# Kernel optimization log

Hardware: AMD Instinct MI355X
Metric: run time of the kernel (lower is better)

Reference implementation:

```python
import jax, jax.numpy as jnp
import numpy as np
from jax import lax

NUM_HEADS = 6
LN_EPS = 1e-5


def _ln(x, g, b):
    mu = jnp.mean(x, axis=-1, keepdims=True)
    var = jnp.mean(jnp.square(x - mu), axis=-1, keepdims=True)
    return (x - mu) * jax.lax.rsqrt(var + LN_EPS) * g + b


def _gelu(x):
    return jax.nn.gelu(x, approximate=False)


def setup_inputs() -> dict:
    key = jax.random.key(0)
    ks = jax.random.split(key, 16)
    B, N, C = 16, 1025, 384
    hid = 4 * C  # 1536
    k3 = 3  # depthwise kernel size
    s = 0.02
    rn = lambda k, shape: (jax.random.normal(k, shape, jnp.float32) * s)
    return {
        "x": jax.random.normal(ks[0], (B, N, C), jnp.float32),
        "ln1_g": jnp.ones((C,), jnp.float32),
        "ln1_b": jnp.zeros((C,), jnp.float32),
        "qkv_w": rn(ks[1], (3 * C, C)),
        "proj_w": rn(ks[2], (C, C)),
        "proj_b": jnp.zeros((C,), jnp.float32),
        "ln2_g": jnp.ones((C,), jnp.float32),
        "ln2_b": jnp.zeros((C,), jnp.float32),
        "conv1_w": rn(ks[3], (hid, C)),          # 1x1 conv as matrix
        "conv1_b": jnp.zeros((hid,), jnp.float32),
        "conv2_w": rn(ks[4], (hid, 1, k3, k3)),   # depthwise OIHW
        "conv2_b": jnp.zeros((hid,), jnp.float32),
        "conv3_w": rn(ks[5], (C, hid)),           # 1x1 conv as matrix
        "conv3_b": jnp.zeros((C,), jnp.float32),
        "bn1_s": jnp.ones((hid,), jnp.float32), "bn1_b": jnp.zeros((hid,), jnp.float32),
        "bn2_s": jnp.ones((hid,), jnp.float32), "bn2_b": jnp.zeros((hid,), jnp.float32),
        "bn3_s": jnp.ones((C,), jnp.float32), "bn3_b": jnp.zeros((C,), jnp.float32),
        "comp_w": rn(ks[6], (C // 4, C)), "comp_b": jnp.zeros((C // 4,), jnp.float32),
        "exc_w": rn(ks[7], (C, C // 4)), "exc_b": jnp.zeros((C,), jnp.float32),
    }


def _block(x, ln1_g, ln1_b, qkv_w, proj_w, proj_b, ln2_g, ln2_b,
           conv1_w, conv1_b, conv2_w, conv2_b, conv3_w, conv3_b,
           bn1_s, bn1_b, bn2_s, bn2_b, bn3_s, bn3_b,
           comp_w, comp_b, exc_w, exc_b):
    B, N, C = x.shape
    Hh = NUM_HEADS
    hd = C // Hh
    S = int(np.sqrt(N - 1))

    # ---- Attention (manual softmax(QK^T)V) ----
    h = _ln(x, ln1_g, ln1_b)
    qkv = jnp.einsum('bnc,dc->bnd', h, qkv_w).reshape(B, N, 3, Hh, hd)
    qkv = qkv.transpose(2, 0, 3, 1, 4)  # [3,B,H,N,hd]
    q, k, v = qkv[0], qkv[1], qkv[2]
    attn = jax.nn.softmax(jnp.einsum('bhqd,bhkd->bhqk', q, k) * (hd ** -0.5), axis=-1)
    o = jnp.einsum('bhqk,bhkd->bhqd', attn, v).transpose(0, 2, 1, 3).reshape(B, N, C)
    o = o @ proj_w.T + proj_b
    x = x + o

    # ---- DAFF FFN (conv + BN(eval affine) + GELU + SE gating on cls) ----
    h2 = _ln(x, ln2_g, ln2_b)
    cls_tok, tok = h2[:, :1], h2[:, 1:]
    t = tok.reshape(B, S, S, C).transpose(0, 3, 1, 2)  # NCHW
    hid = conv1_w.shape[0]
    y = jnp.einsum('bchw,oc->bohw', t, conv1_w) + conv1_b[None, :, None, None]
    y = y * bn1_s[None, :, None, None] + bn1_b[None, :, None, None]
    y = _gelu(y)
    shortcut = y
    y = lax.conv_general_dilated(y, conv2_w, (1, 1), 'SAME',
                                 feature_group_count=hid,
                                 dimension_numbers=('NCHW', 'OIHW', 'NCHW'))
    y = y + conv2_b[None, :, None, None]
    y = y * bn2_s[None, :, None, None] + bn2_b[None, :, None, None]
    y = shortcut + _gelu(y)
    y = jnp.einsum('bchw,oc->bohw', y, conv3_w) + conv3_b[None, :, None, None]
    y = y * bn3_s[None, :, None, None] + bn3_b[None, :, None, None]
    # SE gate on cls token
    w = jnp.mean(y, axis=(2, 3)).reshape(B, 1, C)
    w = _gelu(w @ comp_w.T + comp_b) @ exc_w.T + exc_b
    cls_out = cls_tok * w
    tok_out = y.reshape(B, C, S * S).transpose(0, 2, 1)
    out = jnp.concatenate([cls_out, tok_out], axis=1)
    return x + out


def reference(x, ln1_g, ln1_b, qkv_w, proj_w, proj_b, ln2_g, ln2_b,
              conv1_w, conv1_b, conv2_w, conv2_b, conv3_w, conv3_b,
              bn1_s, bn1_b, bn2_s, bn2_b, bn3_s, bn3_b,
              comp_w, comp_b, exc_w, exc_b):
    return _block(x, ln1_g, ln1_b, qkv_w, proj_w, proj_b, ln2_g, ln2_b,
                  conv1_w, conv1_b, conv2_w, conv2_b, conv3_w, conv3_b,
                  bn1_s, bn1_b, bn2_s, bn2_b, bn3_s, bn3_b,
                  comp_w, comp_b, exc_w, exc_b)
```

## Files before the change

### kernel.cpp

```cpp
#include <hip/hip_runtime.h>
#include <math.h>

#define DI __device__ __forceinline__

namespace {

constexpr int B_ = 16;
constexpr int N_ = 1025;
constexpr int C_ = 384;
constexpr int H_ = 6;
constexpr int HD_ = 64;
constexpr int HID_ = 1536;
constexpr int P_ = 1024;
constexpr int MTOK = B_ * P_;
constexpr int MALL = B_ * N_;
constexpr int NPAD = 1088;
constexpr long long AF = (long long)MALL * C_;

constexpr int NQKV = 3 * C_ * C_;
constexpr int NPROJ = C_ * C_;
constexpr int NC1 = HID_ * C_;
constexpr int NC3 = C_ * HID_;
constexpr int NW2 = HID_ * 9;
constexpr int T1 = NQKV, T2 = T1 + NPROJ, T3 = T2 + NC1, T4 = T3 + NC3;
constexpr int T5 = T4 + NW2, T6 = T5 + HID_;

typedef __attribute__((ext_vector_type(4))) float f32x4;
typedef __attribute__((ext_vector_type(16))) float f32x16;
typedef __attribute__((ext_vector_type(8))) short bf16x8;

DI float gelu_f(float x) { return 0.5f * x * (1.0f + erff(x * 0.7071067811865475f)); }

DI float us2f(unsigned short u) {
  union { unsigned int i; float f; } c; c.i = ((unsigned)u) << 16; return c.f;
}
DI unsigned short f2us(float f) {
  union { float f; unsigned int i; } c; c.f = f;
  unsigned int r = c.i + 0x7FFF + ((c.i >> 16) & 1);
  return (unsigned short)(r >> 16);
}
DI unsigned short f2us_trunc(float f) {
  union { float f; unsigned int i; } c; c.f = f;
  return (unsigned short)(c.i >> 16);
}
DI void bf8_to_f(const uint4 v, float* f) {
  const unsigned int u[4] = {v.x, v.y, v.z, v.w};
#pragma unroll
  for (int t = 0; t < 4; t++) {
    union { unsigned int i; float fl; } lo, hi;
    lo.i = (u[t] & 0xffffu) << 16;
    hi.i = u[t] & 0xffff0000u;
    f[2 * t] = lo.fl; f[2 * t + 1] = hi.fl;
  }
}
DI uint4 f_to_bf8(const float* f) {
  unsigned int w[4];
#pragma unroll
  for (int t = 0; t < 4; t++)
    w[t] = (unsigned)f2us(f[2 * t]) | ((unsigned)f2us(f[2 * t + 1]) << 16);
  return make_uint4(w[0], w[1], w[2], w[3]);
}

DI unsigned cvt_pk_bf16(float lo, float hi) {
  unsigned d;
  asm("v_cvt_pk_bf16_f32 %0, %1, %2" : "=v"(d) : "v"(lo), "v"(hi));
  return d;
}
DI void permswap(unsigned &a, unsigned &b) {
  asm("v_permlane32_swap_b32 %0, %1" : "+v"(a), "+v"(b));
}

DI void gl2lds16(const unsigned short* g, unsigned short* l) {
  __builtin_amdgcn_global_load_lds(
      (const __attribute__((address_space(1))) void*)g,
      (__attribute__((address_space(3))) void*)l, 16, 0, 0);
}

__global__ __launch_bounds__(256) void cvtall_kernel(
    const float* __restrict__ qkv_w, const float* __restrict__ proj_w,
    const float* __restrict__ conv1_w, const float* __restrict__ conv3_w,
    const float* __restrict__ conv2_w, const float* __restrict__ c2b,
    const float* __restrict__ s2, const float* __restrict__ b2,
    unsigned short* __restrict__ dst16, float* __restrict__ Bc)
{
  const int idx = blockIdx.x * 256 + threadIdx.x;
  if (idx < T1)      dst16[idx] = f2us(qkv_w[idx]);
  else if (idx < T2) dst16[idx] = f2us(proj_w[idx - T1]);
  else if (idx < T3) dst16[idx] = f2us(conv1_w[idx - T2]);
  else if (idx < T4) dst16[idx] = f2us(conv3_w[idx - T3]);
  else if (idx < T5) {
    const int r = idx - T4, tap = r / HID_, c = r % HID_;
    dst16[idx] = f2us(conv2_w[c * 9 + tap] * s2[c]);
  } else if (idx < T6) {
    const int c = idx - T5;
    Bc[c] = c2b[c] * s2[c] + b2[c];
  }
}

__global__ __launch_bounds__(256) void lnw_kernel(
    const float* __restrict__ x, const float* __restrict__ g,
    const float* __restrict__ b, unsigned short* __restrict__ out,
    float* __restrict__ cls_out, int nrows)
{
  const int row = blockIdx.x * 4 + (threadIdx.x >> 6);
  if (row >= nrows) return;
  const int lane = threadIdx.x & 63;
  const float* xr = x + (long long)row * C_;
  float v[6];
#pragma unroll
  for (int i = 0; i < 6; i++) v[i] = xr[lane + 64 * i];
  float s = 0.f, q = 0.f;
#pragma unroll
  for (int i = 0; i < 6; i++) { s += v[i]; q += v[i] * v[i]; }
#pragma unroll
  for (int m = 1; m < 64; m <<= 1) {
    s += __shfl_xor(s, m, 64);
    q += __shfl_xor(q, m, 64);
  }
  const float mean = s * (1.0f / C_);
  const float var  = q * (1.0f / C_) - mean * mean;
  const float rstd = rsqrtf(var + 1e-5f);
  unsigned short* orow = out + (long long)row * C_;
  const bool iscls = (cls_out != nullptr) && (row % N_) == 0;
  float* cr = iscls ? cls_out + (long long)(row / N_) * C_ : nullptr;
#pragma unroll
  for (int i = 0; i < 6; i++) {
    const int c = lane + 64 * i;
    const float r = (v[i] - mean) * rstd * g[c] + b[c];
    orow[c] = f2us(r);
    if (iscls) cr[c] = r;
  }
}

__global__ __launch_bounds__(256) void vtrans_kernel(
    const unsigned short* __restrict__ v, unsigned short* __restrict__ vt)
{
  __shared__ unsigned short t[64][72];
  const int bh = blockIdx.x, nt = blockIdx.y;
  const int n0 = nt * 64;
  const int tid = threadIdx.x;
  {
    const int nl = tid >> 2;
    const int dc = (tid & 3) * 16;
    const int gn = n0 + nl;
    uint4 a = make_uint4(0u,0u,0u,0u), b = make_uint4(0u,0u,0u,0u);
    if (gn < N_) {
      const unsigned short* p = v + ((long long)bh * N_ + gn) * HD_ + dc;
      a = *(const uint4*)p; b = *(const uint4*)(p + 8);
    }
    *(uint4*)&t[nl][dc] = a;
    *(uint4*)&t[nl][dc + 8] = b;
  }
  __syncthreads();
  {
    const int dl = tid >> 2;
    const int nc = (tid & 3) * 16;
    unsigned short tmp[16];
#pragma unroll
    for (int i = 0; i < 16; i++) tmp[i] = t[nc + i][dl];
    unsigned short* p = vt + ((long long)bh * HD_ + dl) * NPAD + n0 + nc;
    *(uint4*)p = *(uint4*)&tmp[0];
    *(uint4*)(p + 8) = *(uint4*)&tmp[8];
  }
}

enum { GM_QKV = 0, GM_PROJ = 1, GM_CONV1 = 2, GM_CONV3 = 3 };

template <int MODE, int K>
__global__ __launch_bounds__(256) void mgemm_kernel(
    const unsigned short* __restrict__ A, const unsigned short* __restrict__ W,
    void* __restrict__ o0, void* __restrict__ o1, void* __restrict__ o2,
    const float* __restrict__ e0, const float* __restrict__ e1,
    const float* __restrict__ e2, int M)
{
  __shared__ unsigned short As[2][128][64];
  __shared__ unsigned short Bs[2][128][64];
  const int m0 = blockIdx.x * 128, n0 = blockIdx.y * 128;
  if (m0 >= M) return;
  const int tid = threadIdx.x;
  const int lane = tid & 63, wv = tid >> 6;
  const int lane15 = lane & 15, quad = lane >> 4;
  const int wm = (wv >> 1) * 64, wn = (wv & 1) * 64;

  const unsigned short* agp[4];
  const unsigned short* bgp[4];
#pragma unroll
  for (int t = 0; t < 4; t++) {
    const int lr = wv * 32 + t * 8 + (lane >> 3);
    const int chunk = (lane & 7) ^ (lr & 7);
    int gm = m0 + lr;
    if (gm > M - 1) gm = M - 1;
    long long arow = gm;
    if constexpr (MODE == GM_CONV1) arow = (long long)(gm >> 10) * N_ + 1 + (gm & 1023);
    agp[t] = A + arow * K + chunk * 8;
    bgp[t] = W + (long long)(n0 + lr) * K + chunk * 8;
  }

  f32x4 acc[4][4];
#pragma unroll
  for (int i = 0; i < 4; i++)
#pragma unroll
    for (int j = 0; j < 4; j++) acc[i][j] = (f32x4)0.f;

  const int xsel = lane15 & 7;
  constexpr int NT = K / 64;

#pragma unroll
  for (int t = 0; t < 4; t++) {
    gl2lds16(agp[t], &As[0][wv * 32 + t * 8][0]);
    gl2lds16(bgp[t], &Bs[0][wv * 32 + t * 8][0]);
  }

  for (int it = 0; it < NT; ++it) {
    const int cur = it & 1;
    if (it + 1 < NT) {
      const int k0 = (it + 1) * 64;
#pragma unroll
      for (int t = 0; t < 4; t++) {
        gl2lds16(agp[t] + k0, &As[cur ^ 1][wv * 32 + t * 8][0]);
        gl2lds16(bgp[t] + k0, &Bs[cur ^ 1][wv * 32 + t * 8][0]);
      }
      asm volatile("s_waitcnt vmcnt(8)" ::: "memory");
    } else {
      asm volatile("s_waitcnt vmcnt(0)" ::: "memory");
    }
    asm volatile("s_barrier" ::: "memory");
    __builtin_amdgcn_sched_barrier(0);
#pragma unroll
    for (int kh = 0; kh < 2; kh++) {
      bf16x8 af[4], bfr[4];
#pragma unroll
      for (int i = 0; i < 4; i++)
        af[i] = *(const bf16x8*)&As[cur][wm + i * 16 + lane15][((kh * 4 + quad) ^ xsel) * 8];
#pragma unroll
      for (int j = 0; j < 4; j++)
        bfr[j] = *(const bf16x8*)&Bs[cur][wn + j * 16 + lane15][((kh * 4 + quad) ^ xsel) * 8];
#pragma unroll
      for (int i = 0; i < 4; i++)
#pragma unroll
        for (int j = 0; j < 4; j++)
          acc[i][j] = __builtin_amdgcn_mfma_f32_16x16x32_bf16(af[i], bfr[j], acc[i][j], 0, 0, 0);
    }
    asm volatile("s_barrier" ::: "memory");
  }
#pragma unroll
  for (int i = 0; i < 4; i++) {
#pragma unroll
    for (int r = 0; r < 4; r++) {
      const int m = m0 + wm + i * 16 + quad * 4 + r;
      if (m >= M) continue;
#pragma unroll
      for (int j = 0; j < 4; j++) {
        const int n = n0 + wn + j * 16 + lane15;
        const float val = acc[i][j][r];
        if constexpr (MODE == GM_QKV) {
          const int which = n / C_, rr = n % C_, hh = rr >> 6, e = rr & 63;
          const int b = m / N_, nn = m % N_;
          unsigned short* dst = (unsigned short*)((which == 0) ? o0 : ((which == 1) ? o1 : o2));
          const float sval = (which == 0) ? val * 0.18033688f : val;
          dst[(((long long)b * H_ + hh) * N_ + nn) * HD_ + e] = f2us(sval);
        } else if constexpr (MODE == GM_PROJ) {
          ((float*)o0)[(long long)m * C_ + n] = val + e0[(long long)m * C_ + n] + e1[n];
        } else if constexpr (MODE == GM_CONV1) {
          ((unsigned short*)o0)[(long long)m * HID_ + n] =
              f2us(gelu_f((val + e0[n]) * e1[n] + e2[n]));
        } else {
          const float val2 = (val + e0[n]) * e1[n] + e2[n];
          ((float*)o0)[(long long)m * C_ + n] = val2;
          const int bb = m >> 10, pp = m & 1023;
          const long long orow = ((long long)bb * N_ + 1 + pp) * C_ + n;
          ((float*)o1)[orow] = ((const float*)o2)[orow] + val2;
        }
      }
    }
  }
}

__global__ __launch_bounds__(512) void fattn_kernel(
    const unsigned short* __restrict__ q, const unsigned short* __restrict__ k,
    const unsigned short* __restrict__ vt, unsigned short* __restrict__ o)
{
  __shared__ unsigned short smem[32768];
  const int tid = threadIdx.x;
  const int lane = tid & 63, wv = tid >> 6;
  const int qw = wv & 3, kg = wv >> 2;
  const int lane31 = lane & 31, half = lane >> 5;
  const int x7 = lane & 7;
  const int bh = blockIdx.x, qt = blockIdx.y;
  const long long headoff = (long long)bh * N_;
  const int q0w = qt * 128 + qw * 32;
  const bool active = q0w < N_;
  const int nreal = kg ? 8 : 9;
  const int kbase = kg * 576;

  unsigned short* Ksm = smem;
  unsigned short* Vsm = smem + 16384;

  int gq = q0w + lane31; if (gq > N_ - 1) gq = N_ - 1;
  const unsigned short* qp = q + (headoff + gq) * HD_ + half * 8;
  bf16x8 qf[4];
#pragma unroll
  for (int m = 0; m < 4; m++) qf[m] = *(const bf16x8*)(qp + m * 16);

  const unsigned short* kgp[2];
  const unsigned short* vgp[2];
#pragma unroll
  for (int t = 0; t < 2; t++) {
    const int r = t * 32 + qw * 8 + (lane >> 3);
    const int ch = (lane & 7) ^ (r & 7);
    kgp[t] = k + (headoff + kbase + r) * HD_ + ch * 8;
    vgp[t] = vt + ((long long)bh * HD_ + r) * NPAD + kbase + ch * 8;
  }

  f32x16 O0 = (f32x16)0.f, O1 = (f32x16)0.f;
  float l = 0.f;

#pragma unroll
  for (int t = 0; t < 2; t++) {
    gl2lds16(kgp[t], Ksm + (kg * 2 + 0) * 4096 + (t * 32 + qw * 8) * 64);
    gl2lds16(vgp[t], Vsm + (kg * 2 + 0) * 4096 + (t * 32 + qw * 8) * 64);
  }
  __syncthreads();

  for (int it = 0; it < 9; it++) {
    const int cur = it & 1;
    if (it + 1 < nreal) {
      const long long koff = (long long)(it + 1) * 64;
#pragma unroll
      for (int t = 0; t < 2; t++) {
        gl2lds16(kgp[t] + koff * HD_,
                 Ksm + (kg * 2 + (cur ^ 1)) * 4096 + (t * 32 + qw * 8) * 64);
        gl2lds16(vgp[t] + koff,
                 Vsm + (kg * 2 + (cur ^ 1)) * 4096 + (t * 32 + qw * 8) * 64);
      }
    }
    if (active && it < nreal) {
      const unsigned short* Kb = Ksm + (kg * 2 + cur) * 4096;
      const unsigned short* Vb = Vsm + (kg * 2 + cur) * 4096;
      f32x16 S0 = (f32x16)0.f, S1 = (f32x16)0.f;
      __builtin_amdgcn_s_setprio(1);
#pragma unroll
      for (int m = 0; m < 4; m++) {
        const int chs = ((m * 2 + half) ^ x7) * 8;
        const bf16x8 k0 = *(const bf16x8*)&Kb[lane31 * 64 + chs];
        const bf16x8 k1 = *(const bf16x8*)&Kb[(32 + lane31) * 64 + chs];
        S0 = __builtin_amdgcn_mfma_f32_32x32x16_bf16(k0, qf[m], S0, 0, 0, 0);
        S1 = __builtin_amdgcn_mfma_f32_32x32x16_bf16(k1, qf[m], S1, 0, 0, 0);
      }
      __builtin_amdgcn_s_setprio(0);
      if (kg == 1 && it == 7) {
#pragma unroll
        for (int r = 0; r < 16; r++) {
          const int kl = (r & 3) + 8 * (r >> 2) + 4 * half;
          if (1024 + kl >= N_) S0[r] = -1e30f;
          S1[r] = -1e30f;
        }
      }
      unsigned pk0[8], pk1[8];
#pragma unroll
      for (int s = 0; s < 8; s++) {
        const float a0 = exp2f(S0[2 * s]), a1 = exp2f(S0[2 * s + 1]);
        const float b0 = exp2f(S1[2 * s]), b1 = exp2f(S1[2 * s + 1]);
        l += (a0 + a1) + (b0 + b1);
        pk0[s] = cvt_pk_bf16(a0, a1);
        pk1[s] = cvt_pk_bf16(b0, b1);
      }
      unsigned wkc[4][4];
#pragma unroll
      for (int bb = 0; bb < 2; bb++) {
#pragma unroll
        for (int kc2 = 0; kc2 < 2; kc2++) {
          unsigned a0 = bb ? pk1[kc2 * 4 + 0] : pk0[kc2 * 4 + 0];
          unsigned a2 = bb ? pk1[kc2 * 4 + 2] : pk0[kc2 * 4 + 2];
          permswap(a0, a2);
          unsigned a1 = bb ? pk1[kc2 * 4 + 1] : pk0[kc2 * 4 + 1];
          unsigned a3 = bb ? pk1[kc2 * 4 + 3] : pk0[kc2 * 4 + 3];
          permswap(a1, a3);
          const int kc = bb * 2 + kc2;
          wkc[kc][0] = a0; wkc[kc][1] = a1; wkc[kc][2] = a2; wkc[kc][3] = a3;
        }
      }
      __builtin_amdgcn_s_setprio(1);
#pragma unroll
      for (int kc = 0; kc < 4; kc++) {
        union { unsigned u[4]; bf16x8 v; } pa;
        pa.u[0] = wkc[kc][0]; pa.u[1] = wkc[kc][1];
        pa.u[2] = wkc[kc][2]; pa.u[3] = wkc[kc][3];
        const int chv = ((kc * 2 + half) ^ x7) * 8;
        const bf16x8 v0 = *(const bf16x8*)&Vb[lane31 * 64 + chv];
        const bf16x8 v1 = *(const bf16x8*)&Vb[(32 + lane31) * 64 + chv];
        O0 = __builtin_amdgcn_mfma_f32_32x32x16_bf16(pa.v, v0, O0, 0, 0, 0);
        O1 = __builtin_amdgcn_mfma_f32_32x32x16_bf16(pa.v, v1, O1, 0, 0, 0);
      }
      __builtin_amdgcn_s_setprio(0);
    }
    __syncthreads();
  }

  float* mrg = (float*)smem;
  if (kg == 1 && active) {
    float* mq = mrg + qw * 33 * 64 + lane;
#pragma unroll
    for (int j = 0; j < 16; j++) mq[j * 64] = O0[j];
#pragma unroll
    for (int j = 0; j < 16; j++) mq[(16 + j) * 64] = O1[j];
    mq[32 * 64] = l;
  }
  __syncthreads();
  if (kg == 0 && active) {
    float* mq = mrg + qw * 33 * 64 + lane;
#pragma unroll
    for (int j = 0; j < 16; j++) O0[j] += mq[j * 64];
#pragma unroll
    for (int j = 0; j < 16; j++) O1[j] += mq[(16 + j) * 64];
    l += mq[32 * 64];

    l += __shfl_xor(l, 32, 64);
    const float rinv = 1.0f / l;
    float li[16];
#pragma unroll
    for (int r = 0; r < 16; r++) {
      const int qloc = (r & 3) + 8 * (r >> 2) + 4 * half;
      li[r] = __int_as_float(
          __builtin_amdgcn_ds_bpermute(qloc * 4, __float_as_int(rinv)));
    }
    const int b = bh / H_, hh = bh % H_;
#pragma unroll
    for (int r = 0; r < 16; r++) {
      const int qloc = (r & 3) + 8 * (r >> 2) + 4 * half;
      const int gqr = q0w + qloc;
      if (gqr < N_) {
        const long long orow = ((long long)b * N_ + gqr) * C_ + hh * HD_;
        o[orow + lane31] = f2us(O0[r] * li[r]);
        o[orow + 32 + lane31] = f2us(O1[r] * li[r]);
      }
    }
  }
}

__global__ __launch_bounds__(192) void dwconv_kernel(
    const unsigned short* __restrict__ y1, const unsigned short* __restrict__ w2s,
    const float* __restrict__ Bc, unsigned short* __restrict__ y2)
{
  const int jp = blockIdx.x & 15;
  const int i  = (blockIdx.x >> 4) & 31;
  const int b  = blockIdx.x >> 9;
  const int j0 = jp * 2;
  const int cb = threadIdx.x << 3;

  float wf[9][8];
#pragma unroll
  for (int tap = 0; tap < 9; tap++) {
    const uint4 wv = *(const uint4*)(w2s + tap * HID_ + cb);
    bf8_to_f(wv, wf[tap]);
  }
  float acc0[8] = {}, acc1[8] = {};
  float sh0[8], sh1[8];
#pragma unroll
  for (int di = -1; di <= 1; di++) {
    const int ii = i + di;
    if (ii < 0 || ii > 31) continue;
    const long long rowbase = ((long long)b * P_ + ii * 32) * HID_ + cb;
#pragma unroll
    for (int dj = -1; dj <= 2; dj++) {
      const int jj = j0 + dj;
      if (jj < 0 || jj > 31) continue;
      const uint4 dv = *(const uint4*)(y1 + rowbase + (long long)jj * HID_);
      float df[8]; bf8_to_f(dv, df);
      if (dj <= 1) {
        const int tap = (di + 1) * 3 + (dj + 1);
#pragma unroll
        for (int t = 0; t < 8; t++) acc0[t] += df[t] * wf[tap][t];
      }
      if (dj >= 0) {
        const int tap = (di + 1) * 3 + dj;
#pragma unroll
        for (int t = 0; t < 8; t++) acc1[t] += df[t] * wf[tap][t];
      }
      if (di == 0 && dj == 0) {
#pragma unroll
        for (int t = 0; t < 8; t++) sh0[t] = df[t];
      }
      if (di == 0 && dj == 1) {
#pragma unroll
        for (int t = 0; t < 8; t++) sh1[t] = df[t];
      }
    }
  }
  const float4 bc0 = *(const float4*)(Bc + cb);
  const float4 bc1 = *(const float4*)(Bc + cb + 4);
  const float bcv[8] = {bc0.x, bc0.y, bc0.z, bc0.w, bc1.x, bc1.y, bc1.z, bc1.w};
  float of0[8], of1[8];
#pragma unroll
  for (int t = 0; t < 8; t++) {
    of0[t] = sh0[t] + gelu_f(acc0[t] + bcv[t]);
    of1[t] = sh1[t] + gelu_f(acc1[t] + bcv[t]);
  }
  const long long tok0 = ((long long)b * P_ + i * 32 + j0) * HID_ + cb;
  *(uint4*)(y2 + tok0) = f_to_bf8(of0);
  *(uint4*)(y2 + tok0 + HID_) = f_to_bf8(of1);
}

__global__ __launch_bounds__(384) void pool_kernel(const float* __restrict__ y3,
                                                   float* __restrict__ w0p)
{
  const int b = blockIdx.x, chunk = blockIdx.y;
  const int c = threadIdx.x;
  float s = 0.f;
  for (int p = chunk * 64; p < chunk * 64 + 64; p++)
    s += y3[((long long)b * P_ + p) * C_ + c];
  w0p[((long long)b * 16 + chunk) * C_ + c] = s;
}

__global__ __launch_bounds__(128) void se_kernel(
    const float* __restrict__ w0p, const float* __restrict__ cw,
    const float* __restrict__ cb, const float* __restrict__ ew,
    const float* __restrict__ eb, float* __restrict__ wfin)
{
  __shared__ float wm[384];
  __shared__ float t1[96];
  const int b = blockIdx.x, t = threadIdx.x;
  for (int c = t; c < 384; c += 128) {
    float s = 0.f;
    for (int ch = 0; ch < 16; ch++) s += w0p[((long long)b * 16 + ch) * C_ + c];
    wm[c] = s * (1.0f / 1024.0f);
  }
  __syncthreads();
  if (t < 96) {
    float s = cb[t];
    for (int c = 0; c < 384; c++) s += wm[c] * cw[t * 384 + c];
    t1[t] = gelu_f(s);
  }
  __syncthreads();
  for (int c = t; c < 384; c += 128) {
    float s = eb[c];
    for (int j = 0; j < 96; j++) s += t1[j] * ew[c * 96 + j];
    wfin[(long long)b * C_ + c] = s;
  }
}

__global__ __launch_bounds__(256) void clsfix_kernel(
    const float* __restrict__ x2, const float* __restrict__ cls,
    const float* __restrict__ wfin, float* __restrict__ out)
{
  const int idx = blockIdx.x * 256 + threadIdx.x;
  if (idx >= B_ * C_) return;
  const int b = idx / C_, c = idx % C_;
  const long long row = (long long)b * N_ * C_ + c;
  out[row] = x2[row] + cls[idx] * wfin[idx];
}

}

extern "C" void kernel_launch(void* const* d_in, const int* in_sizes, int n_in,
                              void* d_out, int out_size, void* d_ws, size_t ws_size,
                              hipStream_t stream)
{
  const float* x       = (const float*)d_in[0];
  const float* ln1_g   = (const float*)d_in[1];
  const float* ln1_b   = (const float*)d_in[2];
  const float* qkv_w   = (const float*)d_in[3];
  const float* proj_w  = (const float*)d_in[4];
  const float* proj_b  = (const float*)d_in[5];
  const float* ln2_g   = (const float*)d_in[6];
  const float* ln2_b   = (const float*)d_in[7];
  const float* conv1_w = (const float*)d_in[8];
  const float* conv1_b = (const float*)d_in[9];
  const float* conv2_w = (const float*)d_in[10];
  const float* conv2_b = (const float*)d_in[11];
  const float* conv3_w = (const float*)d_in[12];
  const float* conv3_b = (const float*)d_in[13];
  const float* bn1_s   = (const float*)d_in[14];
  const float* bn1_b   = (const float*)d_in[15];
  const float* bn2_s   = (const float*)d_in[16];
  const float* bn2_b   = (const float*)d_in[17];
  const float* bn3_s   = (const float*)d_in[18];
  const float* bn3_b   = (const float*)d_in[19];
  const float* comp_w  = (const float*)d_in[20];
  const float* comp_b  = (const float*)d_in[21];
  const float* exc_w   = (const float*)d_in[22];
  const float* exc_b   = (const float*)d_in[23];

  char* wsb = (char*)d_ws;
  const size_t RA = 50331648, RB = 50331648, RC = 25190400;
  const size_t tailbytes = (size_t)T5 * 2 +
                           (size_t)(HID_ + B_ * C_ + B_ * 16 * C_ + B_ * C_) * 4;
  const size_t needed = RA + RB + RC + tailbytes;
  if (ws_size < needed) return;

  unsigned short* qb  = (unsigned short*)wsb;
  unsigned short* kb  = qb + AF;
  unsigned short* vb  = kb + AF;
  unsigned short* h2b = (unsigned short*)wsb;
  unsigned short* y2  = (unsigned short*)wsb;
  char* rb = wsb + RA;
  unsigned short* hb  = (unsigned short*)rb;
  unsigned short* o16 = (unsigned short*)rb;
  unsigned short* y1  = (unsigned short*)rb;
  float* y3           = (float*)rb;
  unsigned short* vtb = (unsigned short*)(wsb + RA + RB);
  float* x2 = (float*)(wsb + RA + RB);
  unsigned short* w16 = (unsigned short*)(wsb + RA + RB + RC);
  unsigned short* wqkv16  = w16;
  unsigned short* wproj16 = w16 + T1;
  unsigned short* wc116   = w16 + T2;
  unsigned short* wc316   = w16 + T3;
  unsigned short* w2s     = w16 + T4;
  float* Bc   = (float*)(w16 + T5);
  float* cls  = Bc + HID_;
  float* w0p  = cls + B_ * C_;
  float* wfin = w0p + B_ * 16 * C_;

  cvtall_kernel<<<(T6 + 255) / 256, 256, 0, stream>>>(
      qkv_w, proj_w, conv1_w, conv3_w, conv2_w, conv2_b, bn2_s, bn2_b, w16, Bc);
  lnw_kernel<<<(MALL + 3) / 4, 256, 0, stream>>>(x, ln1_g, ln1_b, hb, nullptr, MALL);
  mgemm_kernel<GM_QKV, 384><<<dim3(136, 9), 256, 0, stream>>>(
      hb, wqkv16, qb, kb, vb, nullptr, nullptr, nullptr, MALL);
  vtrans_kernel<<<dim3(B_ * H_, 17), 256, 0, stream>>>(vb, vtb);
  fattn_kernel<<<dim3(B_ * H_, 9), 512, 0, stream>>>(qb, kb, vtb, o16);
  mgemm_kernel<GM_PROJ, 384><<<dim3(136, 3), 256, 0, stream>>>(
      o16, wproj16, x2, nullptr, nullptr, x, proj_b, nullptr, MALL);
  lnw_kernel<<<(MALL + 3) / 4, 256, 0, stream>>>(x2, ln2_g, ln2_b, h2b, cls, MALL);
  mgemm_kernel<GM_CONV1, 384><<<dim3(128, 12), 256, 0, stream>>>(
      h2b, wc116, y1, nullptr, nullptr, conv1_b, bn1_s, bn1_b, MTOK);
  dwconv_kernel<<<B_ * 32 * 16, 192, 0, stream>>>(y1, w2s, Bc, y2);
  mgemm_kernel<GM_CONV3, 1536><<<dim3(128, 3), 256, 0, stream>>>(
      y2, wc316, y3, (float*)d_out, x2, conv3_b, bn3_s, bn3_b, MTOK);
  pool_kernel<<<dim3(B_, 16), 384, 0, stream>>>(y3, w0p);
  se_kernel<<<B_, 128, 0, stream>>>(w0p, comp_w, comp_b, exc_w, exc_b, wfin);
  clsfix_kernel<<<(B_ * C_ + 255) / 256, 256, 0, stream>>>(x2, cls, wfin, (float*)d_out);
}
```

Before: 455.8 us.

## Load K and V fragments directly from global memory in attention kernel

Removes the double-buffered LDS staging of K and V tiles, along with the per-iteration __syncthreads, from the flash attention kernel. Each wave now reads its MFMA K/V operands straight from global memory and relies on L1/L2 caching across the four query waves that share them. Shared memory drops to only the merge buffer, which may raise occupancy, but global load latency is no longer hidden by prefetch and the same data is fetched redundantly by several waves.

Result: no change. 462.3 us (+1.4%).

```diff
diff --git a/kernel.cpp b/kernel.cpp
--- a/kernel.cpp
+++ b/kernel.cpp
@@ -38,10 +38,6 @@
   union { float f; unsigned int i; } c; c.f = f;
   unsigned int r = c.i + 0x7FFF + ((c.i >> 16) & 1);
   return (unsigned short)(r >> 16);
-}
-DI unsigned short f2us_trunc(float f) {
-  union { float f; unsigned int i; } c; c.f = f;
-  return (unsigned short)(c.i >> 16);
 }
 DI void bf8_to_f(const uint4 v, float* f) {
   const unsigned int u[4] = {v.x, v.y, v.z, v.w};
@@ -280,12 +276,11 @@
     const unsigned short* __restrict__ q, const unsigned short* __restrict__ k,
     const unsigned short* __restrict__ vt, unsigned short* __restrict__ o)
 {
-  __shared__ unsigned short smem[32768];
+  __shared__ float mrg[4 * 33 * 64];
   const int tid = threadIdx.x;
   const int lane = tid & 63, wv = tid >> 6;
   const int qw = wv & 3, kg = wv >> 2;
   const int lane31 = lane & 31, half = lane >> 5;
-  const int x7 = lane & 7;
   const int bh = blockIdx.x, qt = blockIdx.y;
   const long long headoff = (long long)bh * N_;
   const int q0w = qt * 128 + qw * 32;
@@ -293,57 +288,31 @@
   const int nreal = kg ? 8 : 9;
   const int kbase = kg * 576;
 
-  unsigned short* Ksm = smem;
-  unsigned short* Vsm = smem + 16384;
-
-  int gq = q0w + lane31; if (gq > N_ - 1) gq = N_ - 1;
-  const unsigned short* qp = q + (headoff + gq) * HD_ + half * 8;
-  bf16x8 qf[4];
-#pragma unroll
-  for (int m = 0; m < 4; m++) qf[m] = *(const bf16x8*)(qp + m * 16);
-
-  const unsigned short* kgp[2];
-  const unsigned short* vgp[2];
-#pragma unroll
-  for (int t = 0; t < 2; t++) {
-    const int r = t * 32 + qw * 8 + (lane >> 3);
-    const int ch = (lane & 7) ^ (r & 7);
-    kgp[t] = k + (headoff + kbase + r) * HD_ + ch * 8;
-    vgp[t] = vt + ((long long)bh * HD_ + r) * NPAD + kbase + ch * 8;
-  }
-
   f32x16 O0 = (f32x16)0.f, O1 = (f32x16)0.f;
   float l = 0.f;
 
-#pragma unroll
-  for (int t = 0; t < 2; t++) {
-    gl2lds16(kgp[t], Ksm + (kg * 2 + 0) * 4096 + (t * 32 + qw * 8) * 64);
-    gl2lds16(vgp[t], Vsm + (kg * 2 + 0) * 4096 + (t * 32 + qw * 8) * 64);
-  }
-  __syncthreads();
-
-  for (int it = 0; it < 9; it++) {
-    const int cur = it & 1;
-    if (it + 1 < nreal) {
-      const long long koff = (long long)(it + 1) * 64;
-#pragma unroll
-      for (int t = 0; t < 2; t++) {
-        gl2lds16(kgp[t] + koff * HD_,
-                 Ksm + (kg * 2 + (cur ^ 1)) * 4096 + (t * 32 + qw * 8) * 64);
-        gl2lds16(vgp[t] + koff,
-                 Vsm + (kg * 2 + (cur ^ 1)) * 4096 + (t * 32 + qw * 8) * 64);
-      }
-    }
-    if (active && it < nreal) {
-      const unsigned short* Kb = Ksm + (kg * 2 + cur) * 4096;
-      const unsigned short* Vb = Vsm + (kg * 2 + cur) * 4096;
+  if (active) {
+    int gq = q0w + lane31; if (gq > N_ - 1) gq = N_ - 1;
+    const unsigned short* qp = q + (headoff + gq) * HD_ + half * 8;
+    bf16x8 qf[4];
+#pragma unroll
+    for (int m = 0; m < 4; m++) qf[m] = *(const bf16x8*)(qp + m * 16);
+
+    const unsigned short* kp  = k + (headoff + kbase + lane31) * HD_ + half * 8;
+    const unsigned short* kp2 = kp + 32 * HD_;
+    const unsigned short* vp  = vt + ((long long)bh * HD_ + lane31) * NPAD + kbase + half * 8;
+    const unsigned short* vp2 = vp + 32 * NPAD;
+
+    for (int it = 0; it < nreal; it++) {
+      const long long koH = (long long)it * 64 * HD_;
+      const int koV = it * 64;
+
       f32x16 S0 = (f32x16)0.f, S1 = (f32x16)0.f;
       __builtin_amdgcn_s_setprio(1);
 #pragma unroll
       for (int m = 0; m < 4; m++) {
-        const int chs = ((m * 2 + half) ^ x7) * 8;
-        const bf16x8 k0 = *(const bf16x8*)&Kb[lane31 * 64 + chs];
-        const bf16x8 k1 = *(const bf16x8*)&Kb[(32 + lane31) * 64 + chs];
+        const bf16x8 k0 = *(const bf16x8*)(kp + koH + m * 16);
+        const bf16x8 k1 = *(const bf16x8*)(kp2 + koH + m * 16);
         S0 = __builtin_amdgcn_mfma_f32_32x32x16_bf16(k0, qf[m], S0, 0, 0, 0);
         S1 = __builtin_amdgcn_mfma_f32_32x32x16_bf16(k1, qf[m], S1, 0, 0, 0);
       }
@@ -386,18 +355,15 @@
         union { unsigned u[4]; bf16x8 v; } pa;
         pa.u[0] = wkc[kc][0]; pa.u[1] = wkc[kc][1];
         pa.u[2] = wkc[kc][2]; pa.u[3] = wkc[kc][3];
-        const int chv = ((kc * 2 + half) ^ x7) * 8;
-        const bf16x8 v0 = *(const bf16x8*)&Vb[lane31 * 64 + chv];
-        const bf16x8 v1 = *(const bf16x8*)&Vb[(32 + lane31) * 64 + chv];
+        const bf16x8 v0 = *(const bf16x8*)(vp + koV + kc * 16);
+        const bf16x8 v1 = *(const bf16x8*)(vp2 + koV + kc * 16);
         O0 = __builtin_amdgcn_mfma_f32_32x32x16_bf16(pa.v, v0, O0, 0, 0, 0);
         O1 = __builtin_amdgcn_mfma_f32_32x32x16_bf16(pa.v, v1, O1, 0, 0, 0);
       }
       __builtin_amdgcn_s_setprio(0);
     }
-    __syncthreads();
-  }
-
-  float* mrg = (float*)smem;
+  }
+
   if (kg == 1 && active) {
     float* mq = mrg + qw * 33 * 64 + lane;
 #pragma unroll
```

## Single-buffer K/V in flash attention with staggered loads to cut LDS

Applied to the files above, without the earlier changes.

Replaces the double-buffered K/V shared-memory tiles in the attention kernel with single buffers, shrinking LDS from 64KB to about 33KB so more blocks can be resident per CU. Each iteration now loads the next K tile after QK^T finishes and the next V tile after PV finishes, using manual barriers and vmcnt waits to keep the two loads partly overlapped with compute. The aim is to raise occupancy, at the cost of less prefetch slack and an extra barrier per iteration, which could expose load latency.

Measured after the change: 511.6 us. 12.3% more time.

```diff
diff --git a/kernel.cpp b/kernel.cpp
--- a/kernel.cpp
+++ b/kernel.cpp
@@ -38,10 +38,6 @@
   union { float f; unsigned int i; } c; c.f = f;
   unsigned int r = c.i + 0x7FFF + ((c.i >> 16) & 1);
   return (unsigned short)(r >> 16);
-}
-DI unsigned short f2us_trunc(float f) {
-  union { float f; unsigned int i; } c; c.f = f;
-  return (unsigned short)(c.i >> 16);
 }
 DI void bf8_to_f(const uint4 v, float* f) {
   const unsigned int u[4] = {v.x, v.y, v.z, v.w};
@@ -280,7 +276,9 @@
     const unsigned short* __restrict__ q, const unsigned short* __restrict__ k,
     const unsigned short* __restrict__ vt, unsigned short* __restrict__ o)
 {
-  __shared__ unsigned short smem[32768];
+  __shared__ float mrg[4 * 33 * 64];
+  unsigned short* Ksm = (unsigned short*)mrg;
+  unsigned short* Vsm = Ksm + 8192;
   const int tid = threadIdx.x;
   const int lane = tid & 63, wv = tid >> 6;
   const int qw = wv & 3, kg = wv >> 2;
@@ -293,8 +291,8 @@
   const int nreal = kg ? 8 : 9;
   const int kbase = kg * 576;
 
-  unsigned short* Ksm = smem;
-  unsigned short* Vsm = smem + 16384;
+  unsigned short* Kb = Ksm + kg * 4096;
+  unsigned short* Vb = Vsm + kg * 4096;
 
   int gq = q0w + lane31; if (gq > N_ - 1) gq = N_ - 1;
   const unsigned short* qp = q + (headoff + gq) * HD_ + half * 8;
@@ -316,28 +314,15 @@
   float l = 0.f;
 
 #pragma unroll
-  for (int t = 0; t < 2; t++) {
-    gl2lds16(kgp[t], Ksm + (kg * 2 + 0) * 4096 + (t * 32 + qw * 8) * 64);
-    gl2lds16(vgp[t], Vsm + (kg * 2 + 0) * 4096 + (t * 32 + qw * 8) * 64);
-  }
+  for (int t = 0; t < 2; t++) gl2lds16(kgp[t], Kb + (t * 32 + qw * 8) * 64);
+#pragma unroll
+  for (int t = 0; t < 2; t++) gl2lds16(vgp[t], Vb + (t * 32 + qw * 8) * 64);
   __syncthreads();
 
   for (int it = 0; it < 9; it++) {
-    const int cur = it & 1;
-    if (it + 1 < nreal) {
-      const long long koff = (long long)(it + 1) * 64;
-#pragma unroll
-      for (int t = 0; t < 2; t++) {
-        gl2lds16(kgp[t] + koff * HD_,
-                 Ksm + (kg * 2 + (cur ^ 1)) * 4096 + (t * 32 + qw * 8) * 64);
-        gl2lds16(vgp[t] + koff,
-                 Vsm + (kg * 2 + (cur ^ 1)) * 4096 + (t * 32 + qw * 8) * 64);
-      }
-    }
-    if (active && it < nreal) {
-      const unsigned short* Kb = Ksm + (kg * 2 + cur) * 4096;
-      const unsigned short* Vb = Vsm + (kg * 2 + cur) * 4096;
-      f32x16 S0 = (f32x16)0.f, S1 = (f32x16)0.f;
+    const bool docomp = active && it < nreal;
+    f32x16 S0 = (f32x16)0.f, S1 = (f32x16)0.f;
+    if (docomp) {
       __builtin_amdgcn_s_setprio(1);
 #pragma unroll
       for (int m = 0; m < 4; m++) {
@@ -348,6 +333,15 @@
         S1 = __builtin_amdgcn_mfma_f32_32x32x16_bf16(k1, qf[m], S1, 0, 0, 0);
       }
       __builtin_amdgcn_s_setprio(0);
+    }
+    __syncthreads();
+    if (it + 1 < nreal) {
+      const long long koH = (long long)(it + 1) * 64 * HD_;
+#pragma unroll
+      for (int t = 0; t < 2; t++)
+        gl2lds16(kgp[t] + koH, Kb + (t * 32 + qw * 8) * 64);
+    }
+    if (docomp) {
       if (kg == 1 && it == 7) {
 #pragma unroll
         for (int r = 0; r < 16; r++) {
@@ -394,10 +388,19 @@
       }
       __builtin_amdgcn_s_setprio(0);
     }
-    __syncthreads();
-  }
-
-  float* mrg = (float*)smem;
+    asm volatile("s_barrier" ::: "memory");
+    __builtin_amdgcn_sched_barrier(0);
+    if (it + 1 < nreal) {
+      const int koV = (it + 1) * 64;
+#pragma unroll
+      for (int t = 0; t < 2; t++)
+        gl2lds16(vgp[t] + koV, Vb + (t * 32 + qw * 8) * 64);
+    }
+    asm volatile("s_waitcnt vmcnt(2)" ::: "memory");
+    asm volatile("s_barrier" ::: "memory");
+    __builtin_amdgcn_sched_barrier(0);
+  }
+
   if (kg == 1 && active) {
     float* mq = mrg + qw * 33 * 64 + lane;
 #pragma unroll
```
